# Performance work log

Hardware: AMD Instinct MI355X
Metric: run time of the kernel (lower is better)

## Reference

```python
import jax, jax.numpy as jnp
import numpy as np

B, L, D, H = 4, 2048, 1024, 16
DH = D // H


def setup_inputs() -> dict:
    key = jax.random.key(0)
    ks = jax.random.split(key, 16)
    s = 1.0 / np.sqrt(D)
    return {
        "query": jax.random.normal(ks[0], (B, L, D), jnp.float32),
        "key_": jax.random.normal(ks[1], (B, L, D), jnp.float32),
        "value": jax.random.normal(ks[2], (B, L, D), jnp.float32),
        "mask": jax.random.randint(ks[3], (B, L), 0, 2, jnp.int32),
        "Wq": jax.random.normal(ks[4], (D, D), jnp.float32) * s,
        "bq": jnp.zeros((D,), jnp.float32),
        "Wk": jax.random.normal(ks[5], (D, D), jnp.float32) * s,
        "bk": jnp.zeros((D,), jnp.float32),
        "Wv": jax.random.normal(ks[6], (D, D), jnp.float32) * s,
        "bv": jnp.zeros((D,), jnp.float32),
        "Wo": jax.random.normal(ks[7], (D, D), jnp.float32) * s,
        "bo": jnp.zeros((D,), jnp.float32),
        "gamma": jnp.ones((D,), jnp.float32),
        "beta": jnp.zeros((D,), jnp.float32),
    }


def reference(query, key_, value, mask, Wq, bq, Wk, bk, Wv, bv, Wo, bo, gamma, beta):
    old_query = query
    # projections (Linear: x @ W^T + b)
    q = query @ Wq.T + bq            # [B,L,D]
    k = key_ @ Wk.T + bk
    v = value @ Wv.T + bv
    # split heads -> [B,H,L,DH]
    q = q.reshape(B, L, H, DH).transpose(0, 2, 1, 3)
    k = k.reshape(B, L, H, DH).transpose(0, 2, 1, 3)
    v = v.reshape(B, L, H, DH).transpose(0, 2, 1, 3)
    scores = jnp.einsum("bhqd,bhkd->bhqk", q, k) / jnp.sqrt(jnp.float32(DH))
    m = mask[:, None, None, :]        # [B,1,1,L]
    scores = jnp.where(m == 0, jnp.float32(-1e9), scores)
    attn = jax.nn.softmax(scores, axis=-1)
    out = jnp.einsum("bhqk,bhkd->bhqd", attn, v)
    out = out.transpose(0, 2, 1, 3).reshape(B, L, D)
    out = out @ Wo.T + bo
    # dropout is identity in eval; residual + layernorm (eps=1e-5)
    x = out + old_query
    mu = jnp.mean(x, axis=-1, keepdims=True)
    var = jnp.var(x, axis=-1, keepdims=True)
    return (x - mu) / jnp.sqrt(var + 1e-5) * gamma + beta
```

## Files before the change

kernel.cpp:

```cpp
#include <hip/hip_runtime.h>
#include <hip/hip_bf16.h>

typedef __attribute__((ext_vector_type(4))) float f32x4;
typedef __attribute__((ext_vector_type(16))) float f32x16;
typedef __attribute__((ext_vector_type(2))) unsigned int u32x2;
typedef __attribute__((ext_vector_type(4))) unsigned int u32x4;
typedef __attribute__((ext_vector_type(8))) __bf16 bf16x8;

__device__ inline unsigned short f2bf(float x) {
    return __builtin_bit_cast(unsigned short, (__bf16)x);
}
__device__ inline unsigned int pack2(float lo, float hi) {
    return (unsigned int)f2bf(lo) | ((unsigned int)f2bf(hi) << 16);
}
__device__ inline u32x4 cvt8(const float* __restrict__ p) {
    f32x4 a = *(const f32x4*)p;
    f32x4 b = *(const f32x4*)(p + 4);
    u32x4 r;
    r[0] = pack2(a[0], a[1]);
    r[1] = pack2(a[2], a[3]);
    r[2] = pack2(b[0], b[1]);
    r[3] = pack2(b[2], b[3]);
    return r;
}
__device__ inline bf16x8 ldfrag(const unsigned short* p) {
    u32x4 t = *(const u32x4*)p;
    return __builtin_bit_cast(bf16x8, t);
}

__global__ __launch_bounds__(256) void cvt_bf16(
    const float* __restrict__ src, unsigned short* __restrict__ dst, int n8)
{
    for (int i = blockIdx.x * 256 + threadIdx.x; i < n8; i += gridDim.x * 256)
        *(u32x4*)(dst + (size_t)i * 8) = cvt8(src + (size_t)i * 8);
}
__global__ __launch_bounds__(256) void cvt_w3(
    const float* __restrict__ wq, const float* __restrict__ wk,
    const float* __restrict__ wv, unsigned short* __restrict__ dst)
{
    const float* s = blockIdx.y == 0 ? wq : (blockIdx.y == 1 ? wk : wv);
    unsigned short* d = dst + (size_t)blockIdx.y * 1048576;
    const int i = blockIdx.x * 256 + threadIdx.x;
    *(u32x4*)(d + (size_t)i * 8) = cvt8(s + (size_t)i * 8);
}

__global__ __launch_bounds__(256) void gemm_qkv(
    const float* __restrict__ Aq, const float* __restrict__ Ak,
    const float* __restrict__ Av, const unsigned short* __restrict__ W16,
    const float* __restrict__ bq, const float* __restrict__ bk,
    const float* __restrict__ bv, unsigned short* __restrict__ Qb,
    unsigned short* __restrict__ Kb, unsigned short* __restrict__ Vtb,
    float qscale)
{
    __shared__ unsigned short Al[2][128][40];
    __shared__ unsigned short Bl[2][128][32];
    const int z = blockIdx.x;
    const float* Ap = z == 0 ? Aq : (z == 1 ? Ak : Av);
    const unsigned short* Bw = W16 + (size_t)z * 1048576;
    const float* bias = z == 0 ? bq : (z == 1 ? bk : bv);
    const float alpha = z == 0 ? qscale : 1.0f;

    const int tid = threadIdx.x;
    const int lane = tid & 63, w = tid >> 6;
    const int wr = w >> 1, wc = w & 1;
    const int m0 = blockIdx.y * 128, n0 = blockIdx.z * 128;
    const int fr = lane & 15, fq = lane >> 4;

    f32x4 acc[4][4] = {};
    f32x4 apre[2][2];

    auto issueB = [&](int p, int k0) {
#pragma unroll
        for (int j = 0; j < 2; ++j) {
            const int f = (w * 2 + j) * 512 + lane * 8;
            const int r = f >> 5, c = f & 31;
            __builtin_amdgcn_global_load_lds(
                (const __attribute__((address_space(1))) void*)(Bw + (size_t)(n0 + r) * 1024 + k0 + c),
                (__attribute__((address_space(3))) void*)(&Bl[p][0][0] + (w * 2 + j) * 512),
                16, 0, 0);
        }
    };
    auto issueA = [&](int k0) {
#pragma unroll
        for (int i = 0; i < 2; ++i) {
            const int e = (i * 256 + tid) * 8;
            const int r = e >> 5, c = e & 31;
            const float* src = Ap + (size_t)(m0 + r) * 1024 + k0 + c;
            apre[i][0] = *(const f32x4*)src;
            apre[i][1] = *(const f32x4*)(src + 4);
        }
    };

    issueA(0);
    issueB(0, 0);

    for (int k0 = 0; k0 < 1024; k0 += 32) {
        const int p = (k0 >> 5) & 1;
#pragma unroll
        for (int i = 0; i < 2; ++i) {
            const int e = (i * 256 + tid) * 8;
            const int r = e >> 5, c = e & 31;
            u32x4 v;
            v[0] = pack2(apre[i][0][0], apre[i][0][1]);
            v[1] = pack2(apre[i][0][2], apre[i][0][3]);
            v[2] = pack2(apre[i][1][0], apre[i][1][1]);
            v[3] = pack2(apre[i][1][2], apre[i][1][3]);
            *(u32x4*)&Al[p][r][c] = v;
        }
        __syncthreads();
        if (k0 + 32 < 1024) {
            issueA(k0 + 32);
            issueB(p ^ 1, k0 + 32);
        }

        bf16x8 af[4], bfv[4];
#pragma unroll
        for (int mt = 0; mt < 4; ++mt)
            af[mt] = ldfrag(&Al[p][wr * 64 + mt * 16 + fr][8 * fq]);
#pragma unroll
        for (int nt = 0; nt < 4; ++nt)
            bfv[nt] = ldfrag(&Bl[p][wc * 64 + nt * 16 + fr][8 * fq]);
#pragma unroll
        for (int mt = 0; mt < 4; ++mt)
#pragma unroll
            for (int nt = 0; nt < 4; ++nt)
                acc[mt][nt] = __builtin_amdgcn_mfma_f32_16x16x32_bf16(af[mt], bfv[nt], acc[mt][nt], 0, 0, 0);
    }

#pragma unroll
    for (int mt = 0; mt < 4; ++mt) {
#pragma unroll
        for (int nt = 0; nt < 4; ++nt) {
            const int col = n0 + wc * 64 + nt * 16 + fr;
            const float bb = bias[col];
            const int row0 = m0 + wr * 64 + mt * 16 + fq * 4;
            if (z == 2) {
                float v0 = acc[mt][nt][0] + bb, v1 = acc[mt][nt][1] + bb;
                float v2 = acc[mt][nt][2] + bb, v3 = acc[mt][nt][3] + bb;
                const int bb_ = row0 >> 11, key = row0 & 2047;
                const int key2 = (key & ~12) | ((key & 4) << 1) | ((key & 8) >> 1);
                const size_t idx = ((size_t)bb_ * 1024 + col) * 2048 + key2;
                u32x2 pv;
                pv[0] = pack2(v0, v1);
                pv[1] = pack2(v2, v3);
                *(u32x2*)(Vtb + idx) = pv;
            } else {
                unsigned short* Cb = z == 0 ? Qb : Kb;
#pragma unroll
                for (int r = 0; r < 4; ++r) {
                    const size_t idx = (size_t)(row0 + r) * 1024 + col;
                    Cb[idx] = f2bf((acc[mt][nt][r] + bb) * alpha);
                }
            }
        }
    }
}

__global__ __launch_bounds__(256) void gemm_out(
    const unsigned short* __restrict__ A, const unsigned short* __restrict__ Bw,
    const float* __restrict__ bias, const float* __restrict__ resid,
    float* __restrict__ Cp)
{
    __shared__ unsigned short Al[2][128][32];
    __shared__ unsigned short Bl[2][128][32];
    const int tid = threadIdx.x;
    const int lane = tid & 63, w = tid >> 6;
    const int wr = w >> 1, wc = w & 1;
    const int m0 = blockIdx.x * 128, n0 = blockIdx.y * 128;
    const int fr = lane & 15, fq = lane >> 4;

    f32x4 acc[4][4] = {};

    auto stage = [&](int p, int k0) {
#pragma unroll
        for (int j = 0; j < 2; ++j) {
            const int f = (w * 2 + j) * 512 + lane * 8;
            const int r = f >> 5, c = f & 31;
            __builtin_amdgcn_global_load_lds(
                (const __attribute__((address_space(1))) void*)(A + (size_t)(m0 + r) * 1024 + k0 + c),
                (__attribute__((address_space(3))) void*)(&Al[p][0][0] + (w * 2 + j) * 512),
                16, 0, 0);
            __builtin_amdgcn_global_load_lds(
                (const __attribute__((address_space(1))) void*)(Bw + (size_t)(n0 + r) * 1024 + k0 + c),
                (__attribute__((address_space(3))) void*)(&Bl[p][0][0] + (w * 2 + j) * 512),
                16, 0, 0);
        }
    };

    stage(0, 0);

    for (int k0 = 0; k0 < 1024; k0 += 32) {
        const int p = (k0 >> 5) & 1;
        __syncthreads();
        if (k0 + 32 < 1024) stage(p ^ 1, k0 + 32);

        bf16x8 af[4], bfv[4];
#pragma unroll
        for (int mt = 0; mt < 4; ++mt)
            af[mt] = ldfrag(&Al[p][wr * 64 + mt * 16 + fr][8 * fq]);
#pragma unroll
        for (int nt = 0; nt < 4; ++nt)
            bfv[nt] = ldfrag(&Bl[p][wc * 64 + nt * 16 + fr][8 * fq]);
#pragma unroll
        for (int mt = 0; mt < 4; ++mt)
#pragma unroll
            for (int nt = 0; nt < 4; ++nt)
                acc[mt][nt] = __builtin_amdgcn_mfma_f32_16x16x32_bf16(af[mt], bfv[nt], acc[mt][nt], 0, 0, 0);
    }

#pragma unroll
    for (int mt = 0; mt < 4; ++mt) {
#pragma unroll
        for (int nt = 0; nt < 4; ++nt) {
            const int col = n0 + wc * 64 + nt * 16 + fr;
            const float bb = bias[col];
            const int row0 = m0 + wr * 64 + mt * 16 + fq * 4;
#pragma unroll
            for (int r = 0; r < 4; ++r) {
                const size_t idx = (size_t)(row0 + r) * 1024 + col;
                Cp[idx] = acc[mt][nt][r] + bb + resid[idx];
            }
        }
    }
}

__global__ __launch_bounds__(256, 2) void attn_fwd(
    const unsigned short* __restrict__ Q, const unsigned short* __restrict__ K,
    const unsigned short* __restrict__ Vt_g, const int* __restrict__ mask,
    unsigned short* __restrict__ O)
{
    __shared__ unsigned short Kl[2][64][64];
    __shared__ unsigned short Vl[2][64][64];
    __shared__ unsigned short mlb[2][64];
    const int tid = threadIdx.x, lane = tid & 63, w = tid >> 6;
    const int l31 = lane & 31, hi = lane >> 5;
    const int qb = blockIdx.y >> 3;
    const int bh = ((blockIdx.y & 7) << 3) | blockIdx.x;
    const int q0 = qb * 256;
    const int b = bh >> 4;
    const size_t rowbase = (size_t)b * 2048;
    const int hoff = (bh & 15) * 64;
    const size_t vbase = (size_t)bh * 64 * 2048;

    const u32x4 onesu = {0x3F803F80u, 0x3F803F80u, 0x3F803F80u, 0x3F803F80u};
    const bf16x8 vones = __builtin_bit_cast(bf16x8, onesu);

    const int sw0 = (((l31) ^ (l31 >> 3)) & 7) << 3;
    const int sw1 = (((l31) ^ ((l31 >> 3) + 4)) & 7) << 3;

    bf16x8 aq[2][4];
#pragma unroll
    for (int a = 0; a < 2; ++a) {
        const unsigned short* qp = Q + (rowbase + q0 + w * 64 + a * 32 + l31) * 1024 + hoff + hi * 8;
#pragma unroll
        for (int kk = 0; kk < 4; ++kk) aq[a][kk] = ldfrag(qp + kk * 16);
    }
    f32x16 o[2][2] = {};
    f32x16 os[2] = {};

    int srow[2], scol[2];
#pragma unroll
    for (int i = 0; i < 2; ++i) {
        int e = (i * 256 + tid) * 8;
        srow[i] = e >> 6;
        scol[i] = e & 63;
    }

    u32x4 kpre[2], vpre[2];
    int mpre = 0;
#pragma unroll
    for (int i = 0; i < 2; ++i) {
        kpre[i] = *(const u32x4*)(K + (rowbase + srow[i]) * 1024 + hoff + scol[i]);
        vpre[i] = *(const u32x4*)(Vt_g + vbase + (size_t)srow[i] * 2048 + scol[i]);
    }
    if (tid < 64) mpre = mask[rowbase + tid];

    for (int kb = 0, it = 0; kb < 2048; kb += 64, ++it) {
        const int p = it & 1;
#pragma unroll
        for (int i = 0; i < 2; ++i) {
            const int cs = scol[i] ^ (((srow[i] ^ (srow[i] >> 3)) & 7) << 3);
            *(u32x4*)&Kl[p][srow[i]][cs] = kpre[i];
            *(u32x4*)&Vl[p][srow[i]][cs] = vpre[i];
        }
        if (tid < 64) mlb[p][tid] = f2bf(mpre == 0 ? -30000.0f : 0.0f);
        if (kb + 64 < 2048) {
#pragma unroll
            for (int i = 0; i < 2; ++i) {
                kpre[i] = *(const u32x4*)(K + (rowbase + kb + 64 + srow[i]) * 1024 + hoff + scol[i]);
                vpre[i] = *(const u32x4*)(Vt_g + vbase + (size_t)srow[i] * 2048 + kb + 64 + scol[i]);
            }
            if (tid < 64) mpre = mask[rowbase + kb + 64 + tid];
        }
        __syncthreads();

#pragma unroll
        for (int t = 0; t < 2; ++t) {
            const int swt = t ? sw1 : sw0;
            const unsigned int mv = (hi == 0) ? (unsigned int)mlb[p][t * 32 + l31] : 0u;
            const u32x4 mfu = {mv, 0u, 0u, 0u};
            const bf16x8 kfm = __builtin_bit_cast(bf16x8, mfu);

            f32x16 z0 = {}, z1 = {};
            __builtin_amdgcn_s_setprio(1);
            z0 = __builtin_amdgcn_mfma_f32_32x32x16_bf16(kfm, vones, z0, 0, 0, 0);
            z1 = __builtin_amdgcn_mfma_f32_32x32x16_bf16(kfm, vones, z1, 0, 0, 0);
#pragma unroll
            for (int kk = 0; kk < 4; ++kk) {
                bf16x8 kf = ldfrag(&Kl[p][t * 32 + l31][(kk * 16 + hi * 8) ^ swt]);
                z0 = __builtin_amdgcn_mfma_f32_32x32x16_bf16(kf, aq[0][kk], z0, 0, 0, 0);
                z1 = __builtin_amdgcn_mfma_f32_32x32x16_bf16(kf, aq[1][kk], z1, 0, 0, 0);
            }
            __builtin_amdgcn_s_setprio(0);

            unsigned int pk[2][4][2];
#pragma unroll
            for (int g = 0; g < 4; ++g) {
                {
                    float p0 = __builtin_amdgcn_exp2f(z0[g * 4 + 0]);
                    float p1 = __builtin_amdgcn_exp2f(z0[g * 4 + 1]);
                    float p2 = __builtin_amdgcn_exp2f(z0[g * 4 + 2]);
                    float p3 = __builtin_amdgcn_exp2f(z0[g * 4 + 3]);
                    pk[0][g][0] = pack2(p0, p1);
                    pk[0][g][1] = pack2(p2, p3);
                }
                {
                    float p0 = __builtin_amdgcn_exp2f(z1[g * 4 + 0]);
                    float p1 = __builtin_amdgcn_exp2f(z1[g * 4 + 1]);
                    float p2 = __builtin_amdgcn_exp2f(z1[g * 4 + 2]);
                    float p3 = __builtin_amdgcn_exp2f(z1[g * 4 + 3]);
                    pk[1][g][0] = pack2(p0, p1);
                    pk[1][g][1] = pack2(p2, p3);
                }
            }

#pragma unroll
            for (int half = 0; half < 2; ++half) {
                const int c = t * 2 + half, G = half * 2;
                u32x4 fu0 = {pk[0][G][0], pk[0][G][1], pk[0][G + 1][0], pk[0][G + 1][1]};
                u32x4 fu1 = {pk[1][G][0], pk[1][G][1], pk[1][G + 1][0], pk[1][G + 1][1]};
                bf16x8 pf0 = __builtin_bit_cast(bf16x8, fu0);
                bf16x8 pf1 = __builtin_bit_cast(bf16x8, fu1);
                __builtin_amdgcn_s_setprio(1);
#pragma unroll
                for (int dt = 0; dt < 2; ++dt) {
                    const int swd = dt ? sw1 : sw0;
                    bf16x8 vb = ldfrag(&Vl[p][dt * 32 + l31][(c * 16 + hi * 8) ^ swd]);
                    o[0][dt] = __builtin_amdgcn_mfma_f32_32x32x16_bf16(pf0, vb, o[0][dt], 0, 0, 0);
                    o[1][dt] = __builtin_amdgcn_mfma_f32_32x32x16_bf16(pf1, vb, o[1][dt], 0, 0, 0);
                }
                os[0] = __builtin_amdgcn_mfma_f32_32x32x16_bf16(pf0, vones, os[0], 0, 0, 0);
                os[1] = __builtin_amdgcn_mfma_f32_32x32x16_bf16(pf1, vones, os[1], 0, 0, 0);
                __builtin_amdgcn_s_setprio(0);
            }
        }
    }

#pragma unroll
    for (int a = 0; a < 2; ++a)
#pragma unroll
        for (int g = 0; g < 4; ++g)
#pragma unroll
            for (int j = 0; j < 4; ++j) {
                const float inv = 1.0f / os[a][g * 4 + j];
                const size_t row = rowbase + q0 + w * 64 + a * 32 + g * 8 + hi * 4 + j;
#pragma unroll
                for (int dt = 0; dt < 2; ++dt)
                    O[row * 1024 + hoff + dt * 32 + l31] = f2bf(o[a][dt][g * 4 + j] * inv);
            }
}

__global__ __launch_bounds__(256) void ln_inplace(
    float* __restrict__ X, const float* __restrict__ gamma, const float* __restrict__ beta)
{
    __shared__ float red[8];
    const int tid = threadIdx.x, lane = tid & 63, w = tid >> 6;
    float* p = X + (size_t)blockIdx.x * 1024;
    f32x4 v = *((const f32x4*)p + tid);
    float s = v[0] + v[1] + v[2] + v[3];
    float s2 = v[0] * v[0] + v[1] * v[1] + v[2] * v[2] + v[3] * v[3];
#pragma unroll
    for (int d = 1; d < 64; d <<= 1) {
        s += __shfl_xor(s, d);
        s2 += __shfl_xor(s2, d);
    }
    if (lane == 0) { red[w] = s; red[4 + w] = s2; }
    __syncthreads();
    s = red[0] + red[1] + red[2] + red[3];
    s2 = red[4] + red[5] + red[6] + red[7];
    const float mu = s * (1.0f / 1024.0f);
    const float var = s2 * (1.0f / 1024.0f) - mu * mu;
    const float rstd = rsqrtf(var + 1e-5f);
    f32x4 g = *((const f32x4*)gamma + tid);
    f32x4 be = *((const f32x4*)beta + tid);
    f32x4 out;
#pragma unroll
    for (int j = 0; j < 4; ++j) out[j] = (v[j] - mu) * rstd * g[j] + be[j];
    *((f32x4*)p + tid) = out;
}

extern "C" void kernel_launch(void* const* d_in, const int* in_sizes, int n_in,
                              void* d_out, int out_size, void* d_ws, size_t ws_size,
                              hipStream_t stream) {
    const float* query = (const float*)d_in[0];
    const float* key_  = (const float*)d_in[1];
    const float* value = (const float*)d_in[2];
    const int*   mask  = (const int*)d_in[3];
    const float* Wq = (const float*)d_in[4];
    const float* bq = (const float*)d_in[5];
    const float* Wk = (const float*)d_in[6];
    const float* bk = (const float*)d_in[7];
    const float* Wv = (const float*)d_in[8];
    const float* bv = (const float*)d_in[9];
    const float* Wo = (const float*)d_in[10];
    const float* bo = (const float*)d_in[11];
    const float* gamma = (const float*)d_in[12];
    const float* beta  = (const float*)d_in[13];

    const size_t MD = (size_t)8192 * 1024;
    unsigned short* Qb  = (unsigned short*)d_ws;
    unsigned short* Kb  = Qb + MD;
    unsigned short* Vtb = Kb + MD;
    unsigned short* Ab  = Vtb + MD;
    float* out = (float*)d_out;
    unsigned short* W16 = (unsigned short*)d_out;
    unsigned short* Wo16 = Vtb;

    const float qscale = 0.125f * 1.4426950408889634f;

    cvt_w3<<<dim3(512, 3), 256, 0, stream>>>(Wq, Wk, Wv, W16);
    gemm_qkv<<<dim3(3, 64, 8), 256, 0, stream>>>(
        query, key_, value, W16, bq, bk, bv, Qb, Kb, Vtb, qscale);

    attn_fwd<<<dim3(8, 64), 256, 0, stream>>>(Qb, Kb, Vtb, mask, Ab);

    cvt_bf16<<<512, 256, 0, stream>>>(Wo, Wo16, 131072);
    gemm_out<<<dim3(64, 8), 256, 0, stream>>>(Ab, Wo16, bo, query, out);
    ln_inplace<<<8192, 256, 0, stream>>>(out, gamma, beta);
}
```

Before: 239.6 us.

## Pre-swizzle K/V in QKV GEMM and stream attention tiles via direct LDS loads

Measured after the change: 234.2 us. 1.02x faster.

```diff
diff --git a/kernel.cpp b/kernel.cpp
--- a/kernel.cpp
+++ b/kernel.cpp
@@ -54,7 +54,7 @@
 {
     __shared__ unsigned short Al[2][128][40];
     __shared__ unsigned short Bl[2][128][32];
-    const int z = blockIdx.x;
+    const int z = blockIdx.z;
     const float* Ap = z == 0 ? Aq : (z == 1 ? Ak : Av);
     const unsigned short* Bw = W16 + (size_t)z * 1048576;
     const float* bias = z == 0 ? bq : (z == 1 ? bk : bv);
@@ -63,7 +63,7 @@
     const int tid = threadIdx.x;
     const int lane = tid & 63, w = tid >> 6;
     const int wr = w >> 1, wc = w & 1;
-    const int m0 = blockIdx.y * 128, n0 = blockIdx.z * 128;
+    const int m0 = blockIdx.x * 128, n0 = blockIdx.y * 128;
     const int fr = lane & 15, fq = lane >> 4;
 
     f32x4 acc[4][4] = {};
@@ -139,17 +139,27 @@
                 float v2 = acc[mt][nt][2] + bb, v3 = acc[mt][nt][3] + bb;
                 const int bb_ = row0 >> 11, key = row0 & 2047;
                 const int key2 = (key & ~12) | ((key & 4) << 1) | ((key & 8) >> 1);
-                const size_t idx = ((size_t)bb_ * 1024 + col) * 2048 + key2;
+                const int dh = col & 63;
+                const int gg = ((dh ^ (dh >> 3)) & 7) << 3;
+                const size_t idx = ((size_t)bb_ * 1024 + col) * 2048 + (key2 ^ gg);
                 u32x2 pv;
                 pv[0] = pack2(v0, v1);
                 pv[1] = pack2(v2, v3);
                 *(u32x2*)(Vtb + idx) = pv;
+            } else if (z == 1) {
+#pragma unroll
+                for (int r = 0; r < 4; ++r) {
+                    const int row = row0 + r;
+                    const int tm = row & 127;
+                    const int gg = ((tm ^ (tm >> 3)) & 7) << 3;
+                    const size_t idx = (size_t)row * 1024 + ((col & ~63) | ((col & 63) ^ gg));
+                    Kb[idx] = f2bf(acc[mt][nt][r] + bb);
+                }
             } else {
-                unsigned short* Cb = z == 0 ? Qb : Kb;
 #pragma unroll
                 for (int r = 0; r < 4; ++r) {
                     const size_t idx = (size_t)(row0 + r) * 1024 + col;
-                    Cb[idx] = f2bf((acc[mt][nt][r] + bb) * alpha);
+                    Qb[idx] = f2bf((acc[mt][nt][r] + bb) * alpha);
                 }
             }
         }
@@ -225,13 +235,13 @@
 }
 
 __global__ __launch_bounds__(256, 2) void attn_fwd(
-    const unsigned short* __restrict__ Q, const unsigned short* __restrict__ K,
+    const unsigned short* __restrict__ K, const unsigned short* __restrict__ Q,
     const unsigned short* __restrict__ Vt_g, const int* __restrict__ mask,
     unsigned short* __restrict__ O)
 {
-    __shared__ unsigned short Kl[2][64][64];
-    __shared__ unsigned short Vl[2][64][64];
-    __shared__ unsigned short mlb[2][64];
+    __shared__ unsigned short Kl[2][128][64];
+    __shared__ unsigned short Vl[2][64][128];
+    __shared__ unsigned short mlb[2][128];
     const int tid = threadIdx.x, lane = tid & 63, w = tid >> 6;
     const int l31 = lane & 31, hi = lane >> 5;
     const int qb = blockIdx.y >> 3;
@@ -245,9 +255,6 @@
     const u32x4 onesu = {0x3F803F80u, 0x3F803F80u, 0x3F803F80u, 0x3F803F80u};
     const bf16x8 vones = __builtin_bit_cast(bf16x8, onesu);
 
-    const int sw0 = (((l31) ^ (l31 >> 3)) & 7) << 3;
-    const int sw1 = (((l31) ^ ((l31 >> 3) + 4)) & 7) << 3;
-
     bf16x8 aq[2][4];
 #pragma unroll
     for (int a = 0; a < 2; ++a) {
@@ -258,45 +265,39 @@
     f32x16 o[2][2] = {};
     f32x16 os[2] = {};
 
-    int srow[2], scol[2];
-#pragma unroll
-    for (int i = 0; i < 2; ++i) {
-        int e = (i * 256 + tid) * 8;
-        srow[i] = e >> 6;
-        scol[i] = e & 63;
-    }
-
-    u32x4 kpre[2], vpre[2];
-    int mpre = 0;
-#pragma unroll
-    for (int i = 0; i < 2; ++i) {
-        kpre[i] = *(const u32x4*)(K + (rowbase + srow[i]) * 1024 + hoff + scol[i]);
-        vpre[i] = *(const u32x4*)(Vt_g + vbase + (size_t)srow[i] * 2048 + scol[i]);
-    }
-    if (tid < 64) mpre = mask[rowbase + tid];
-
-    for (int kb = 0, it = 0; kb < 2048; kb += 64, ++it) {
+    auto stageKV = [&](int p, int kb2) {
+#pragma unroll
+        for (int j = 0; j < 4; ++j) {
+            const int q = w * 4 + j;
+            const int hK = q * 512 + lane * 8;
+            const int rK = hK >> 6, cK = hK & 63;
+            __builtin_amdgcn_global_load_lds(
+                (const __attribute__((address_space(1))) void*)(K + (rowbase + kb2 + rK) * 1024 + hoff + cK),
+                (__attribute__((address_space(3))) void*)(&Kl[p][0][0] + q * 512),
+                16, 0, 0);
+            const int rV = hK >> 7, cV = hK & 127;
+            __builtin_amdgcn_global_load_lds(
+                (const __attribute__((address_space(1))) void*)(Vt_g + vbase + (size_t)rV * 2048 + kb2 + cV),
+                (__attribute__((address_space(3))) void*)(&Vl[p][0][0] + q * 512),
+                16, 0, 0);
+        }
+    };
+
+    stageKV(0, 0);
+    int mpre = (tid < 128) ? mask[rowbase + tid] : 0;
+    if (tid < 128) mlb[0][tid] = f2bf(mpre == 0 ? -30000.0f : 0.0f);
+    __syncthreads();
+
+    for (int kb = 0, it = 0; kb < 2048; kb += 128, ++it) {
         const int p = it & 1;
-#pragma unroll
-        for (int i = 0; i < 2; ++i) {
-            const int cs = scol[i] ^ (((srow[i] ^ (srow[i] >> 3)) & 7) << 3);
-            *(u32x4*)&Kl[p][srow[i]][cs] = kpre[i];
-            *(u32x4*)&Vl[p][srow[i]][cs] = vpre[i];
-        }
-        if (tid < 64) mlb[p][tid] = f2bf(mpre == 0 ? -30000.0f : 0.0f);
-        if (kb + 64 < 2048) {
-#pragma unroll
-            for (int i = 0; i < 2; ++i) {
-                kpre[i] = *(const u32x4*)(K + (rowbase + kb + 64 + srow[i]) * 1024 + hoff + scol[i]);
-                vpre[i] = *(const u32x4*)(Vt_g + vbase + (size_t)srow[i] * 2048 + kb + 64 + scol[i]);
-            }
-            if (tid < 64) mpre = mask[rowbase + kb + 64 + tid];
-        }
-        __syncthreads();
-
-#pragma unroll
-        for (int t = 0; t < 2; ++t) {
-            const int swt = t ? sw1 : sw0;
+        if (kb + 128 < 2048) {
+            stageKV(p ^ 1, kb + 128);
+            if (tid < 128) mpre = mask[rowbase + kb + 128 + tid];
+        }
+
+#pragma unroll
+        for (int t = 0; t < 4; ++t) {
+            const int swt = ((l31 ^ ((l31 >> 3) + t * 4)) & 7) << 3;
             const unsigned int mv = (hi == 0) ? (unsigned int)mlb[p][t * 32 + l31] : 0u;
             const u32x4 mfu = {mv, 0u, 0u, 0u};
             const bf16x8 kfm = __builtin_bit_cast(bf16x8, mfu);
@@ -344,7 +345,7 @@
                 __builtin_amdgcn_s_setprio(1);
 #pragma unroll
                 for (int dt = 0; dt < 2; ++dt) {
-                    const int swd = dt ? sw1 : sw0;
+                    const int swd = ((l31 ^ ((l31 >> 3) + dt * 4)) & 7) << 3;
                     bf16x8 vb = ldfrag(&Vl[p][dt * 32 + l31][(c * 16 + hi * 8) ^ swd]);
                     o[0][dt] = __builtin_amdgcn_mfma_f32_32x32x16_bf16(pf0, vb, o[0][dt], 0, 0, 0);
                     o[1][dt] = __builtin_amdgcn_mfma_f32_32x32x16_bf16(pf1, vb, o[1][dt], 0, 0, 0);
@@ -354,6 +355,10 @@
                 __builtin_amdgcn_s_setprio(0);
             }
         }
+
+        if (kb + 128 < 2048 && tid < 128)
+            mlb[p ^ 1][tid] = f2bf(mpre == 0 ? -30000.0f : 0.0f);
+        __syncthreads();
     }
 
 #pragma unroll
@@ -429,10 +434,10 @@
     const float qscale = 0.125f * 1.4426950408889634f;
 
     cvt_w3<<<dim3(512, 3), 256, 0, stream>>>(Wq, Wk, Wv, W16);
-    gemm_qkv<<<dim3(3, 64, 8), 256, 0, stream>>>(
+    gemm_qkv<<<dim3(64, 8, 3), 256, 0, stream>>>(
         query, key_, value, W16, bq, bk, bv, Qb, Kb, Vtb, qscale);
 
-    attn_fwd<<<dim3(8, 64), 256, 0, stream>>>(Qb, Kb, Vtb, mask, Ab);
+    attn_fwd<<<dim3(8, 64), 256, 0, stream>>>(Kb, Qb, Vtb, mask, Ab);
 
     cvt_bf16<<<512, 256, 0, stream>>>(Wo, Wo16, 131072);
     gemm_out<<<dim3(64, 8), 256, 0, stream>>>(Ab, Wo16, bo, query, out);
```
